# Optimization experiments

Hardware: AMD Instinct MI355X
Metric: run time of the kernel (lower is better)

Reference implementation:

```python
import jax, jax.numpy as jnp
import numpy as np

B = 8192
D = 4096  # input_size == hidden_size (required by the module's forward)
H = 4096


def setup_inputs() -> dict:
    key = jax.random.key(0)
    ks = jax.random.split(key, 14)
    s = 0.02
    inp = {
        "input": jax.random.normal(ks[0], (B, D), dtype=jnp.float32),
        "hidden_state": jax.random.normal(ks[1], (B, H), dtype=jnp.float32),
        # torch nn.Linear weights: [out_features, in_features]
        "w_ir": jax.random.normal(ks[2], (H, D), dtype=jnp.float32) * s,
        "b_ir": jax.random.normal(ks[3], (H,), dtype=jnp.float32) * s,
        "w_iz": jax.random.normal(ks[4], (H, D), dtype=jnp.float32) * s,
        "b_iz": jax.random.normal(ks[5], (H,), dtype=jnp.float32) * s,
        "w_in": jax.random.normal(ks[6], (H, D), dtype=jnp.float32) * s,
        "b_in": jax.random.normal(ks[7], (H,), dtype=jnp.float32) * s,
        "w_hr": jax.random.normal(ks[8], (H, H), dtype=jnp.float32) * s,
        "b_hr": jax.random.normal(ks[9], (H,), dtype=jnp.float32) * s,
        "w_hz": jax.random.normal(ks[10], (H, H), dtype=jnp.float32) * s,
        "b_hz": jax.random.normal(ks[11], (H,), dtype=jnp.float32) * s,
        "w_hn": jax.random.normal(ks[12], (H, H), dtype=jnp.float32) * s,
        "b_hn": jax.random.normal(ks[13], (H,), dtype=jnp.float32) * s,
    }
    return inp


def reference(input, hidden_state, w_ir, b_ir, w_iz, b_iz, w_in, b_in,
              w_hr, b_hr, w_hz, b_hz, w_hn, b_hn):
    # NOTE: faithful to the source: ALL six gates are applied to `input`
    # (the hidden_* gates are also fed `input`, not hidden_state), and the
    # "new" gate uses sigmoid (not tanh).
    # Fuse the six small GEMMs into one batched GEMM: stack weights [6H, D].
    W = jnp.concatenate([w_ir, w_iz, w_in, w_hr, w_hz, w_hn], axis=0)  # [6H, D]
    bvec = jnp.concatenate([b_ir, b_iz, b_in, b_hr, b_hz, b_hn], axis=0)  # [6H]
    g = jnp.einsum('bd,od->bo', input, W) + bvec  # [B, 6H]
    ir, iz, inn, hr, hz, hn = jnp.split(g, 6, axis=-1)
    r = jax.nn.sigmoid(ir + hr)
    z = jax.nn.sigmoid(iz + hz)
    n = jax.nn.sigmoid(inn + r * hn)
    return (1.0 - z) * hidden_state + z * n
```

## Files before the change

### kernel.cpp

```cpp
#include <hip/hip_runtime.h>
#include <hip/hip_bf16.h>


#define THREADS 512
#define B_DIM 8192
#define D_DIM 4096
#define H_DIM 4096
#define BM 256
#define GBN 64
#define BK 64
#define NT (D_DIM / BK)
#define DBUF 65536

#define WS_WR 0
#define WS_WZ 33554432
#define WS_WN 67108864
#define WS_WH 100663296
#define WS_A  134217728
#define WS_NEED 201326592ULL

typedef __attribute__((ext_vector_type(8))) short bf16x8;
typedef __attribute__((ext_vector_type(4))) float f32x4;
typedef __attribute__((ext_vector_type(4))) int i32x4;

__device__ __forceinline__ unsigned f2bf(float f) {
    union { float f; unsigned u; } v; v.f = f;
    return (v.u + 0x7FFFu + ((v.u >> 16) & 1u)) >> 16;
}
__device__ __forceinline__ unsigned pk(float a, float b) {
    return (f2bf(a) & 0xFFFFu) | (f2bf(b) << 16);
}
__device__ __forceinline__ i32x4 pack8(float4 x, float4 y) {
    i32x4 r;
    r[0] = (int)pk(x.x, x.y); r[1] = (int)pk(x.z, x.w);
    r[2] = (int)pk(y.x, y.y); r[3] = (int)pk(y.z, y.w);
    return r;
}
__device__ __forceinline__ float sigmoidf_(float x) {
    return 1.0f / (1.0f + __expf(-x));
}
__device__ __forceinline__ void gld16(const void* g, void* l) {
    __builtin_amdgcn_global_load_lds(
        (const __attribute__((address_space(1))) unsigned*)g,
        (__attribute__((address_space(3))) unsigned*)l, 16, 0, 0);
}

__global__ __launch_bounds__(256) void prep_w_t(
    const float* __restrict__ ir, const float* __restrict__ hr,
    const float* __restrict__ iz, const float* __restrict__ hz,
    const float* __restrict__ inw, const float* __restrict__ hn,
    char* __restrict__ wsbase)
{
    const int tx = threadIdx.x;
    const int R = tx & 15;
    const int c8loc = tx >> 4;
    const int bx = blockIdx.x;
    const int c8blk = bx & 31;
    const int hgrp = bx >> 5;
    const int gy = blockIdx.y;
    const int h  = hgrp * 16 + R;
    const int c8 = c8blk * 16 + c8loc;

    const float* s1 = (gy == 0) ? ir : (gy == 1) ? iz : (gy == 2) ? inw : hn;
    const size_t fi = ((size_t)h * 512 + c8) * 2;
    const float4* p1 = (const float4*)s1;
    float4 a0 = p1[fi], a1 = p1[fi + 1];
    if (gy < 2) {
        const float4* p2 = (const float4*)((gy == 0) ? hr : hz);
        a0 = a0 + p2[fi];
        a1 = a1 + p2[fi + 1];
    }
    const i32x4 v = pack8(a0, a1);
    const int hblk = h >> 6, nfr = (h >> 4) & 3;
    const int t = c8 >> 3, K = (c8 >> 2) & 1, C = c8 & 3;
    const size_t addr = (size_t)gy * 33554432 + (size_t)hblk * 524288
                      + (size_t)t * 8192 + nfr * 2048 + K * 1024 + C * 256 + R * 16;
    *(i32x4*)(wsbase + addr) = v;
}

__global__ __launch_bounds__(256) void prep_a_t(const float* __restrict__ in,
                                                char* __restrict__ abase)
{
    const int tx = threadIdx.x;
    const int R = tx & 15;
    const int c8loc = tx >> 4;
    const int bx = blockIdx.x;
    const int c8blk = bx & 31;
    const int bgrp = bx >> 5;
    const int b  = bgrp * 16 + R;
    const int c8 = c8blk * 16 + c8loc;

    const size_t fi = ((size_t)b * 512 + c8) * 2;
    const float4* p = (const float4*)in;
    const i32x4 v = pack8(p[fi], p[fi + 1]);
    const int bblk = b >> 8, mfr = (b >> 4) & 15;
    const int t = c8 >> 3, K = (c8 >> 2) & 1, C = c8 & 3;
    const size_t addr = (size_t)bblk * 2097152 + (size_t)t * 32768
                      + mfr * 2048 + K * 1024 + C * 256 + R * 16;
    *(i32x4*)(abase + addr) = v;
}

__global__ __launch_bounds__(THREADS, 2) void gru_bf16(
    const char* __restrict__ Abf, const char* __restrict__ Wr,
    const char* __restrict__ Wz, const char* __restrict__ Wn,
    const char* __restrict__ Wh,
    const float* __restrict__ hidden,
    const float* __restrict__ b_ir, const float* __restrict__ b_iz,
    const float* __restrict__ b_in, const float* __restrict__ b_hr,
    const float* __restrict__ b_hz, const float* __restrict__ b_hn,
    float* __restrict__ out)
{
    __shared__ __attribute__((aligned(128))) char smem[2 * DBUF];

    const int tid  = threadIdx.x;
    const int lane = tid & 63;
    const int wid  = tid >> 6;
    const int wm   = wid >> 2;
    const int wn   = wid & 3;

    const int nb   = (int)blockIdx.x;
    const int bblk = nb & 31;
    const int hblk = nb >> 5;
    const int b0 = bblk * BM;
    const int h0 = hblk * GBN;

    const int sg  = wid >> 1;
    const int sn0 = (wid & 1) * 2;
    const char* gWsel = (sg == 0) ? Wr : (sg == 1) ? Wz : (sg == 2) ? Wn : Wh;
    const char* pA = Abf + (size_t)bblk * 2097152 + (size_t)(2 * wid) * 2048 + (lane << 4);
    const char* pB = gWsel + (size_t)hblk * 524288 + (size_t)sn0 * 2048 + (lane << 4);
    const int dA = (2 * wid) * 2048;
    const int dB = 32768 + sg * 8192 + sn0 * 2048;

    f32x4 acc[4][8];
#pragma unroll
    for (int g = 0; g < 4; ++g)
#pragma unroll
        for (int m = 0; m < 8; ++m) acc[g][m] = (f32x4)0.0f;

#define STAGE_A(t, d) do { const size_t ko = (size_t)(t) * 32768;              \
        gld16(pA + ko,        smem + (d) + dA);                                \
        gld16(pA + ko + 1024, smem + (d) + dA + 1024);                         \
        gld16(pA + ko + 2048, smem + (d) + dA + 2048);                         \
        gld16(pA + ko + 3072, smem + (d) + dA + 3072);                         \
    } while (0)

#define STAGE_B(t, d) do { const size_t ko = (size_t)(t) * 8192;               \
        gld16(pB + ko,        smem + (d) + dB);                                \
        gld16(pB + ko + 1024, smem + (d) + dB + 1024);                         \
        gld16(pB + ko + 2048, smem + (d) + dB + 2048);                         \
        gld16(pB + ko + 3072, smem + (d) + dB + 3072);                         \
    } while (0)

#define RD_AF(mhq) do {                                                        \
        _Pragma("unroll")                                                      \
        for (int mf = 0; mf < 4; ++mf)                                         \
            _Pragma("unroll")                                                  \
            for (int kk = 0; kk < 2; ++kk)                                     \
                af[mf][kk] = *(const bf16x8*)(cb + ((wm * 8 + (mhq) * 4 + mf) * 2 + kk) * 1024 + (lane << 4)); \
    } while (0)

#define RD_FB(g) do {                                                          \
        _Pragma("unroll")                                                      \
        for (int kk = 0; kk < 2; ++kk)                                         \
            fb[g][kk] = *(const bf16x8*)(cb + 32768 + (g) * 8192 + (wn * 2 + kk) * 1024 + (lane << 4)); \
    } while (0)

#define MM(acc_, a_, b_) acc_ = __builtin_amdgcn_mfma_f32_16x16x32_bf16(a_, b_, acc_, 0, 0, 0)

#define PH_MFMA(g0_, ab_) do {                                                 \
        __builtin_amdgcn_s_barrier();                                          \
        asm volatile("s_waitcnt lgkmcnt(0)" ::: "memory");                     \
        __builtin_amdgcn_sched_barrier(0);                                     \
        __builtin_amdgcn_s_setprio(1);                                         \
        _Pragma("unroll")                                                      \
        for (int g = (g0_); g < (g0_) + 2; ++g)                                \
            _Pragma("unroll")                                                  \
            for (int mf = 0; mf < 4; ++mf)                                     \
                _Pragma("unroll")                                              \
                for (int kk = 0; kk < 2; ++kk)                                 \
                    MM(acc[g][(ab_) * 4 + mf], af[mf][kk], fb[g][kk]);         \
        __builtin_amdgcn_s_setprio(0);                                         \
    } while (0)

    STAGE_A(0, 0);
    STAGE_B(0, 0);
    asm volatile("s_waitcnt vmcnt(0)" ::: "memory");
    __builtin_amdgcn_s_barrier();

#pragma unroll 1
    for (int t = 0; t < NT; ++t) {
        const int p = t & 1;
        const char* cb = smem + p * DBUF;
        const int d = (p ^ 1) * DBUF;
        const bool stg = (t < NT - 1);
        bf16x8 af[4][2], fb[4][2];

        RD_AF(0);
        RD_FB(0); RD_FB(1);
        if (stg) STAGE_A(t + 1, d);
        PH_MFMA(0, 0);

        RD_FB(2); RD_FB(3);
        if (stg) STAGE_B(t + 1, d);
        PH_MFMA(2, 0);

        RD_AF(1);
        PH_MFMA(0, 1);

        PH_MFMA(2, 1);

        if (stg) { asm volatile("s_waitcnt vmcnt(0)" ::: "memory"); }
        __builtin_amdgcn_s_barrier();
    }

    const int r4 = (lane >> 4) * 4;
    const int cn = lane & 15;
    {
        const int h = h0 + wn * 16 + cn;
        const float br = b_ir[h] + b_hr[h];
        const float bz = b_iz[h] + b_hz[h];
        const float bn = b_in[h];
        const float bh = b_hn[h];
#pragma unroll
        for (int m = 0; m < 8; ++m) {
            const int brow = b0 + wm * 128 + m * 16 + r4;
#pragma unroll
            for (int j = 0; j < 4; ++j) {
                const size_t idx = (size_t)(brow + j) * H_DIM + h;
                const float r = sigmoidf_(acc[0][m][j] + br);
                const float z = sigmoidf_(acc[1][m][j] + bz);
                const float n = sigmoidf_(acc[2][m][j] + bn + r * (acc[3][m][j] + bh));
                out[idx] = (1.0f - z) * hidden[idx] + z * n;
            }
        }
    }
#undef STAGE_A
#undef STAGE_B
#undef RD_AF
#undef RD_FB
#undef MM
#undef PH_MFMA
}

__global__ __launch_bounds__(THREADS, 2) void gru_fused_f32(
    const float* __restrict__ input, const float* __restrict__ hidden,
    const float* __restrict__ w_ir, const float* __restrict__ b_ir,
    const float* __restrict__ w_iz, const float* __restrict__ b_iz,
    const float* __restrict__ w_in, const float* __restrict__ b_in,
    const float* __restrict__ w_hr, const float* __restrict__ b_hr,
    const float* __restrict__ w_hz, const float* __restrict__ b_hz,
    const float* __restrict__ w_hn, const float* __restrict__ b_hn,
    float* __restrict__ out)
{
    __shared__ int smem[2 * 10240];
    const int tid  = threadIdx.x;
    const int lane = tid & 63;
    const int wid  = tid >> 6;
    const int wm   = wid >> 2;
    const int wn   = wid & 3;
    const int bblk = blockIdx.x & 63;
    const int hblk = blockIdx.x >> 6;
    const int b0 = bblk * 128;
    const int h0 = hblk * 128;
    const int srow = tid >> 2;
    const int sc   = tid & 3;
    const float4* gA  = (const float4*)(input + (size_t)(b0 + srow) * D_DIM + sc * 8);
    const size_t woff = (size_t)(h0 + srow) * D_DIM + sc * 8;
    const float4* gIr = (const float4*)(w_ir + woff);
    const float4* gHr = (const float4*)(w_hr + woff);
    const float4* gIz = (const float4*)(w_iz + woff);
    const float4* gHz = (const float4*)(w_hz + woff);
    const float4* gIn = (const float4*)(w_in + woff);
    const float4* gHn = (const float4*)(w_hn + woff);
    const int wr_ints = (srow >> 4) * 256 + ((sc * 16 + (srow & 15)) * 4);

    f32x4 accR[4][2], accZ[4][2], accN[4][2], accH[4][2];
#pragma unroll
    for (int mf = 0; mf < 4; ++mf)
#pragma unroll
        for (int nf = 0; nf < 2; ++nf) {
            accR[mf][nf] = (f32x4)0.0f; accZ[mf][nf] = (f32x4)0.0f;
            accN[mf][nf] = (f32x4)0.0f; accH[mf][nf] = (f32x4)0.0f;
        }
    float4 La0, La1, Lr0, Lr1, Lr2, Lr3, Lz0, Lz1, Lz2, Lz3, Ln0, Ln1, Lh0, Lh1;
#define LOADREGS(s) do { const int o = (s) * 8;                          \
        La0 = gA[o];  La1 = gA[o + 1];                                   \
        Lr0 = gIr[o]; Lr1 = gIr[o + 1]; Lr2 = gHr[o]; Lr3 = gHr[o + 1];  \
        Lz0 = gIz[o]; Lz1 = gIz[o + 1]; Lz2 = gHz[o]; Lz3 = gHz[o + 1];  \
        Ln0 = gIn[o]; Ln1 = gIn[o + 1];                                  \
        Lh0 = gHn[o]; Lh1 = gHn[o + 1]; } while (0)
#define WRITELDS(pp) do { const int wb = (pp) * 10240 + wr_ints;          \
        *(i32x4*)&smem[wb]        = pack8(La0, La1);                      \
        *(i32x4*)&smem[wb + 2048] = pack8(Lr0 + Lr2, Lr1 + Lr3);          \
        *(i32x4*)&smem[wb + 4096] = pack8(Lz0 + Lz2, Lz1 + Lz3);          \
        *(i32x4*)&smem[wb + 6144] = pack8(Ln0, Ln1);                      \
        *(i32x4*)&smem[wb + 8192] = pack8(Lh0, Lh1); } while (0)
#define COMPUTE(pp) do {                                                  \
        const int cb = (pp) * 10240;                                      \
        const bf16x8* Af = (const bf16x8*)&smem[cb];                      \
        const bf16x8* Br = (const bf16x8*)&smem[cb + 2048];               \
        const bf16x8* Bz = (const bf16x8*)&smem[cb + 4096];               \
        const bf16x8* Bn = (const bf16x8*)&smem[cb + 6144];               \
        const bf16x8* Bh = (const bf16x8*)&smem[cb + 8192];               \
        bf16x8 afr[4];                                                    \
        _Pragma("unroll")                                                 \
        for (int mf = 0; mf < 4; ++mf)                                    \
            afr[mf] = Af[(wm * 4 + mf) * 64 + lane];                      \
        _Pragma("unroll")                                                 \
        for (int nf = 0; nf < 2; ++nf) {                                  \
            const int bi = (wn * 2 + nf) * 64 + lane;                     \
            bf16x8 fr = Br[bi], fz = Bz[bi], fn = Bn[bi], fh = Bh[bi];    \
            _Pragma("unroll")                                             \
            for (int mf = 0; mf < 4; ++mf) {                              \
                accR[mf][nf] = __builtin_amdgcn_mfma_f32_16x16x32_bf16(afr[mf], fr, accR[mf][nf], 0, 0, 0); \
                accZ[mf][nf] = __builtin_amdgcn_mfma_f32_16x16x32_bf16(afr[mf], fz, accZ[mf][nf], 0, 0, 0); \
                accN[mf][nf] = __builtin_amdgcn_mfma_f32_16x16x32_bf16(afr[mf], fn, accN[mf][nf], 0, 0, 0); \
                accH[mf][nf] = __builtin_amdgcn_mfma_f32_16x16x32_bf16(afr[mf], fh, accH[mf][nf], 0, 0, 0); \
            }                                                             \
        } } while (0)
    LOADREGS(0);
    WRITELDS(0);
    __syncthreads();
#pragma unroll 1
    for (int s = 0; s < 128; ++s) {
        if (s + 1 < 128) LOADREGS(s + 1);
        COMPUTE(s & 1);
        if (s + 1 < 128) { WRITELDS((s + 1) & 1); __syncthreads(); }
    }
    const int r4 = (lane >> 4) * 4;
    const int cn = lane & 15;
#pragma unroll
    for (int nf = 0; nf < 2; ++nf) {
        const int h = h0 + wn * 32 + nf * 16 + cn;
        const float br = b_ir[h] + b_hr[h];
        const float bz = b_iz[h] + b_hz[h];
        const float bn = b_in[h];
        const float bh = b_hn[h];
#pragma unroll
        for (int mf = 0; mf < 4; ++mf) {
            const int brow = b0 + wm * 64 + mf * 16 + r4;
#pragma unroll
            for (int j = 0; j < 4; ++j) {
                const size_t idx = (size_t)(brow + j) * H_DIM + h;
                const float r = sigmoidf_(accR[mf][nf][j] + br);
                const float z = sigmoidf_(accZ[mf][nf][j] + bz);
                const float n = sigmoidf_(accN[mf][nf][j] + bn + r * (accH[mf][nf][j] + bh));
                out[idx] = (1.0f - z) * hidden[idx] + z * n;
            }
        }
    }
#undef LOADREGS
#undef WRITELDS
#undef COMPUTE
}

extern "C" void kernel_launch(void* const* d_in, const int* in_sizes, int n_in,
                              void* d_out, int out_size, void* d_ws, size_t ws_size,
                              hipStream_t stream) {
    const float* input  = (const float*)d_in[0];
    const float* hidden = (const float*)d_in[1];
    const float* w_ir = (const float*)d_in[2];  const float* b_ir = (const float*)d_in[3];
    const float* w_iz = (const float*)d_in[4];  const float* b_iz = (const float*)d_in[5];
    const float* w_in = (const float*)d_in[6];  const float* b_in = (const float*)d_in[7];
    const float* w_hr = (const float*)d_in[8];  const float* b_hr = (const float*)d_in[9];
    const float* w_hz = (const float*)d_in[10]; const float* b_hz = (const float*)d_in[11];
    const float* w_hn = (const float*)d_in[12]; const float* b_hn = (const float*)d_in[13];
    float* out = (float*)d_out;

    if (ws_size >= WS_NEED) {
        char* ws = (char*)d_ws;
        prep_w_t<<<dim3(8192, 4), dim3(256), 0, stream>>>(
            w_ir, w_hr, w_iz, w_hz, w_in, w_hn, ws);
        prep_a_t<<<dim3(16384), dim3(256), 0, stream>>>(input, ws + WS_A);
        gru_bf16<<<dim3((B_DIM / BM) * (H_DIM / GBN)), dim3(THREADS), 0, stream>>>(
            ws + WS_A, ws + WS_WR, ws + WS_WZ, ws + WS_WN, ws + WS_WH,
            hidden, b_ir, b_iz, b_in, b_hr, b_hz, b_hn, out);
    } else {
        gru_fused_f32<<<dim3(2048), dim3(THREADS), 0, stream>>>(
            input, hidden, w_ir, b_ir, w_iz, b_iz, w_in, b_in,
            w_hr, b_hr, w_hz, b_hz, w_hn, b_hn, out);
    }
}
```

Before: 1.013 ms.

## Remove per-phase barriers and overlap LDS fragment reads with MFMA clusters

Replaces the four barrier-gated MFMA phases per K-tile with a software-pipelined schedule. The second A-fragment half is double-registered (afA/afB) so its LDS reads are issued while the first MFMA cluster runs, and partial lgkmcnt waits replace full barriers plus lgkmcnt(0) before each phase. This cuts intra-iteration workgroup synchronization and exposed LDS latency, at the cost of extra VGPRs for the second A-fragment set, which could pressure occupancy at 2 waves/SIMD.

New measurement: 998.7 us. No clear change (-1.5%).

```diff
diff --git a/kernel.cpp b/kernel.cpp
--- a/kernel.cpp
+++ b/kernel.cpp
@@ -152,12 +152,12 @@
         gld16(pB + ko + 3072, smem + (d) + dB + 3072);                         \
     } while (0)
 
-#define RD_AF(mhq) do {                                                        \
+#define RD_AF(dst, mhq) do {                                                   \
         _Pragma("unroll")                                                      \
         for (int mf = 0; mf < 4; ++mf)                                         \
             _Pragma("unroll")                                                  \
             for (int kk = 0; kk < 2; ++kk)                                     \
-                af[mf][kk] = *(const bf16x8*)(cb + ((wm * 8 + (mhq) * 4 + mf) * 2 + kk) * 1024 + (lane << 4)); \
+                dst[mf][kk] = *(const bf16x8*)(cb + ((wm * 8 + (mhq) * 4 + mf) * 2 + kk) * 1024 + (lane << 4)); \
     } while (0)
 
 #define RD_FB(g) do {                                                          \
@@ -168,10 +168,7 @@
 
 #define MM(acc_, a_, b_) acc_ = __builtin_amdgcn_mfma_f32_16x16x32_bf16(a_, b_, acc_, 0, 0, 0)
 
-#define PH_MFMA(g0_, ab_) do {                                                 \
-        __builtin_amdgcn_s_barrier();                                          \
-        asm volatile("s_waitcnt lgkmcnt(0)" ::: "memory");                     \
-        __builtin_amdgcn_sched_barrier(0);                                     \
+#define MFMA_CL(src, g0_, ab_) do {                                            \
         __builtin_amdgcn_s_setprio(1);                                         \
         _Pragma("unroll")                                                      \
         for (int g = (g0_); g < (g0_) + 2; ++g)                                \
@@ -179,9 +176,11 @@
             for (int mf = 0; mf < 4; ++mf)                                     \
                 _Pragma("unroll")                                              \
                 for (int kk = 0; kk < 2; ++kk)                                 \
-                    MM(acc[g][(ab_) * 4 + mf], af[mf][kk], fb[g][kk]);         \
+                    MM(acc[g][(ab_) * 4 + mf], src[mf][kk], fb[g][kk]);        \
         __builtin_amdgcn_s_setprio(0);                                         \
     } while (0)
+
+#define SB0 __builtin_amdgcn_sched_barrier(0)
 
     STAGE_A(0, 0);
     STAGE_B(0, 0);
@@ -194,23 +193,27 @@
         const char* cb = smem + p * DBUF;
         const int d = (p ^ 1) * DBUF;
         const bool stg = (t < NT - 1);
-        bf16x8 af[4][2], fb[4][2];
-
-        RD_AF(0);
+        bf16x8 afA[4][2], afB[4][2], fb[4][2];
+
+        RD_AF(afA, 0);
         RD_FB(0); RD_FB(1);
         if (stg) STAGE_A(t + 1, d);
-        PH_MFMA(0, 0);
-
+        SB0;
         RD_FB(2); RD_FB(3);
         if (stg) STAGE_B(t + 1, d);
-        PH_MFMA(2, 0);
-
-        RD_AF(1);
-        PH_MFMA(0, 1);
-
-        PH_MFMA(2, 1);
-
+        asm volatile("s_waitcnt lgkmcnt(4)" ::: "memory");
+        SB0;
+        MFMA_CL(afA, 0, 0);
+        asm volatile("s_waitcnt lgkmcnt(0)" ::: "memory");
+        SB0;
+        RD_AF(afB, 1);
+        MFMA_CL(afA, 2, 0);
+        asm volatile("s_waitcnt lgkmcnt(0)" ::: "memory");
+        SB0;
+        MFMA_CL(afB, 0, 1);
+        MFMA_CL(afB, 2, 1);
         if (stg) { asm volatile("s_waitcnt vmcnt(0)" ::: "memory"); }
+        SB0;
         __builtin_amdgcn_s_barrier();
     }
 
@@ -240,7 +243,8 @@
 #undef RD_AF
 #undef RD_FB
 #undef MM
-#undef PH_MFMA
+#undef MFMA_CL
+#undef SB0
 }
 
 __global__ __launch_bounds__(THREADS, 2) void gru_fused_f32(
```

## Use 4-stage LDS ring with BK=32 and register double-buffered fragments

Applied to the files above, without the earlier changes.

Halves the K tile to 32 and replaces the two-buffer LDS scheme with a four-slot ring that prefetches three tiles ahead. Each tile now needs one barrier instead of four. Fragments for the next tile are read into a second register set while the current tile's 32 MFMAs issue. Half the waves now stage A and the other half stage one weight gate each, and the prep kernels are relaid out for the new tile shape. The deeper prefetch is meant to hide global load latency better, at the cost of twice as many loop iterations and extra register pressure from the two fragment sets.

New measurement: 1.023 ms. About the same (+1.0%).

```diff
diff --git a/kernel.cpp b/kernel.cpp
--- a/kernel.cpp
+++ b/kernel.cpp
@@ -8,9 +8,9 @@
 #define H_DIM 4096
 #define BM 256
 #define GBN 64
-#define BK 64
+#define BK 32
 #define NT (D_DIM / BK)
-#define DBUF 65536
+#define TBYTES 32768
 
 #define WS_WR 0
 #define WS_WZ 33554432
@@ -72,9 +72,9 @@
     }
     const i32x4 v = pack8(a0, a1);
     const int hblk = h >> 6, nfr = (h >> 4) & 3;
-    const int t = c8 >> 3, K = (c8 >> 2) & 1, C = c8 & 3;
+    const int t = c8 >> 2, C = c8 & 3;
     const size_t addr = (size_t)gy * 33554432 + (size_t)hblk * 524288
-                      + (size_t)t * 8192 + nfr * 2048 + K * 1024 + C * 256 + R * 16;
+                      + (size_t)t * 4096 + nfr * 1024 + C * 256 + R * 16;
     *(i32x4*)(wsbase + addr) = v;
 }
 
@@ -94,9 +94,9 @@
     const float4* p = (const float4*)in;
     const i32x4 v = pack8(p[fi], p[fi + 1]);
     const int bblk = b >> 8, mfr = (b >> 4) & 15;
-    const int t = c8 >> 3, K = (c8 >> 2) & 1, C = c8 & 3;
-    const size_t addr = (size_t)bblk * 2097152 + (size_t)t * 32768
-                      + mfr * 2048 + K * 1024 + C * 256 + R * 16;
+    const int t = c8 >> 2, C = c8 & 3;
+    const size_t addr = (size_t)bblk * 2097152 + (size_t)t * 16384
+                      + mfr * 1024 + C * 256 + R * 16;
     *(i32x4*)(abase + addr) = v;
 }
 
@@ -110,7 +110,7 @@
     const float* __restrict__ b_hz, const float* __restrict__ b_hn,
     float* __restrict__ out)
 {
-    __shared__ __attribute__((aligned(128))) char smem[2 * DBUF];
+    __shared__ __attribute__((aligned(128))) char smem[4 * TBYTES];
 
     const int tid  = threadIdx.x;
     const int lane = tid & 63;
@@ -124,13 +124,13 @@
     const int b0 = bblk * BM;
     const int h0 = hblk * GBN;
 
-    const int sg  = wid >> 1;
-    const int sn0 = (wid & 1) * 2;
-    const char* gWsel = (sg == 0) ? Wr : (sg == 1) ? Wz : (sg == 2) ? Wn : Wh;
-    const char* pA = Abf + (size_t)bblk * 2097152 + (size_t)(2 * wid) * 2048 + (lane << 4);
-    const char* pB = gWsel + (size_t)hblk * 524288 + (size_t)sn0 * 2048 + (lane << 4);
-    const int dA = (2 * wid) * 2048;
-    const int dB = 32768 + sg * 8192 + sn0 * 2048;
+    const int gg = (wid >= 4) ? (wid - 4) : 0;
+    const char* gW = (gg == 0) ? Wr : (gg == 1) ? Wz : (gg == 2) ? Wn : Wh;
+    const char* psrc = (wid < 4)
+        ? Abf + (size_t)bblk * 2097152 + (size_t)(4 * wid) * 1024 + (lane << 4)
+        : gW + (size_t)hblk * 524288 + (lane << 4);
+    const size_t pstep = (wid < 4) ? 16384 : 4096;
+    const int dst = (wid < 4) ? (4 * wid) * 1024 : (16384 + gg * 4096);
 
     f32x4 acc[4][8];
 #pragma unroll
@@ -138,80 +138,61 @@
 #pragma unroll
         for (int m = 0; m < 8; ++m) acc[g][m] = (f32x4)0.0f;
 
-#define STAGE_A(t, d) do { const size_t ko = (size_t)(t) * 32768;              \
-        gld16(pA + ko,        smem + (d) + dA);                                \
-        gld16(pA + ko + 1024, smem + (d) + dA + 1024);                         \
-        gld16(pA + ko + 2048, smem + (d) + dA + 2048);                         \
-        gld16(pA + ko + 3072, smem + (d) + dA + 3072);                         \
+#define STAGE(x) do {                                                          \
+        const char* s_ = psrc + (size_t)(x) * pstep;                           \
+        char* l_ = smem + ((x) & 3) * TBYTES + dst;                            \
+        gld16(s_, l_); gld16(s_ + 1024, l_ + 1024);                            \
+        gld16(s_ + 2048, l_ + 2048); gld16(s_ + 3072, l_ + 3072);              \
     } while (0)
 
-#define STAGE_B(t, d) do { const size_t ko = (size_t)(t) * 8192;               \
-        gld16(pB + ko,        smem + (d) + dB);                                \
-        gld16(pB + ko + 1024, smem + (d) + dB + 1024);                         \
-        gld16(pB + ko + 2048, smem + (d) + dB + 2048);                         \
-        gld16(pB + ko + 3072, smem + (d) + dB + 3072);                         \
+#define RD(dA_, dF_, x) do {                                                   \
+        const char* cb_ = smem + ((x) & 3) * TBYTES;                           \
+        _Pragma("unroll")                                                      \
+        for (int mf = 0; mf < 8; ++mf)                                         \
+            dA_[mf] = *(const bf16x8*)(cb_ + (wm * 8 + mf) * 1024 + (lane << 4)); \
+        _Pragma("unroll")                                                      \
+        for (int g = 0; g < 4; ++g)                                            \
+            dF_[g] = *(const bf16x8*)(cb_ + 16384 + g * 4096 + wn * 1024 + (lane << 4)); \
     } while (0)
 
-#define RD_AF(mhq) do {                                                        \
-        _Pragma("unroll")                                                      \
-        for (int mf = 0; mf < 4; ++mf)                                         \
-            _Pragma("unroll")                                                  \
-            for (int kk = 0; kk < 2; ++kk)                                     \
-                af[mf][kk] = *(const bf16x8*)(cb + ((wm * 8 + (mhq) * 4 + mf) * 2 + kk) * 1024 + (lane << 4)); \
-    } while (0)
-
-#define RD_FB(g) do {                                                          \
-        _Pragma("unroll")                                                      \
-        for (int kk = 0; kk < 2; ++kk)                                         \
-            fb[g][kk] = *(const bf16x8*)(cb + 32768 + (g) * 8192 + (wn * 2 + kk) * 1024 + (lane << 4)); \
-    } while (0)
-
 #define MM(acc_, a_, b_) acc_ = __builtin_amdgcn_mfma_f32_16x16x32_bf16(a_, b_, acc_, 0, 0, 0)
 
-#define PH_MFMA(g0_, ab_) do {                                                 \
-        __builtin_amdgcn_s_barrier();                                          \
-        asm volatile("s_waitcnt lgkmcnt(0)" ::: "memory");                     \
-        __builtin_amdgcn_sched_barrier(0);                                     \
+#define MFMA32(A_, F_) do {                                                    \
         __builtin_amdgcn_s_setprio(1);                                         \
         _Pragma("unroll")                                                      \
-        for (int g = (g0_); g < (g0_) + 2; ++g)                                \
+        for (int g = 0; g < 4; ++g)                                            \
             _Pragma("unroll")                                                  \
-            for (int mf = 0; mf < 4; ++mf)                                     \
-                _Pragma("unroll")                                              \
-                for (int kk = 0; kk < 2; ++kk)                                 \
-                    MM(acc[g][(ab_) * 4 + mf], af[mf][kk], fb[g][kk]);         \
+            for (int mf = 0; mf < 8; ++mf)                                     \
+                MM(acc[g][mf], A_[mf], F_[g]);                                 \
         __builtin_amdgcn_s_setprio(0);                                         \
     } while (0)
 
-    STAGE_A(0, 0);
-    STAGE_B(0, 0);
-    asm volatile("s_waitcnt vmcnt(0)" ::: "memory");
+#define SB0 __builtin_amdgcn_sched_barrier(0)
+
+#define BODY(t, cA, cF, nA, nF) do {                                           \
+        asm volatile("s_waitcnt lgkmcnt(0)" ::: "memory");                     \
+        SB0;                                                                   \
+        if ((t) + 3 < NT) STAGE((t) + 3);                                      \
+        if ((t) + 1 < NT) RD(nA, nF, (t) + 1);                                 \
+        MFMA32(cA, cF);                                                        \
+        if ((t) <= NT - 4) { asm volatile("s_waitcnt vmcnt(4)" ::: "memory"); }\
+        else               { asm volatile("s_waitcnt vmcnt(0)" ::: "memory"); }\
+        SB0;                                                                   \
+        __builtin_amdgcn_s_barrier();                                          \
+    } while (0)
+
+    bf16x8 a0[8], f0[4], a1[8], f1[4];
+
+    STAGE(0); STAGE(1); STAGE(2);
+    asm volatile("s_waitcnt vmcnt(4)" ::: "memory");
+    SB0;
     __builtin_amdgcn_s_barrier();
+    RD(a0, f0, 0);
 
 #pragma unroll 1
-    for (int t = 0; t < NT; ++t) {
-        const int p = t & 1;
-        const char* cb = smem + p * DBUF;
-        const int d = (p ^ 1) * DBUF;
-        const bool stg = (t < NT - 1);
-        bf16x8 af[4][2], fb[4][2];
-
-        RD_AF(0);
-        RD_FB(0); RD_FB(1);
-        if (stg) STAGE_A(t + 1, d);
-        PH_MFMA(0, 0);
-
-        RD_FB(2); RD_FB(3);
-        if (stg) STAGE_B(t + 1, d);
-        PH_MFMA(2, 0);
-
-        RD_AF(1);
-        PH_MFMA(0, 1);
-
-        PH_MFMA(2, 1);
-
-        if (stg) { asm volatile("s_waitcnt vmcnt(0)" ::: "memory"); }
-        __builtin_amdgcn_s_barrier();
+    for (int t = 0; t < NT; t += 2) {
+        BODY(t,     a0, f0, a1, f1);
+        BODY(t + 1, a1, f1, a0, f0);
     }
 
     const int r4 = (lane >> 4) * 4;
@@ -235,12 +216,12 @@
             }
         }
     }
-#undef STAGE_A
-#undef STAGE_B
-#undef RD_AF
-#undef RD_FB
+#undef STAGE
+#undef RD
 #undef MM
-#undef PH_MFMA
+#undef MFMA32
+#undef SB0
+#undef BODY
 }
 
 __global__ __launch_bounds__(THREADS, 2) void gru_fused_f32(
```
